# Kernel optimization log

Hardware: AMD Instinct MI355X
Metric: run time of the kernel (lower is better)

Reference implementation:

```python
import jax, jax.numpy as jnp
import numpy as np

B, L, D, S = 64, 512, 768, 8
HOP, LAMB = 3, 0.5


def _layernorm(x, g, b, eps=1e-5):
    m = x.mean(-1, keepdims=True)
    v = x.var(-1, keepdims=True)
    return (x - m) / jnp.sqrt(v + eps) * g + b


def _hop_refine(cur, sentence, ln_g, ln_b):
    # cur, sentence: [B,S,D]. HOP-1 refinement steps, then return last row.
    for _ in range(HOP - 1):
        coef = jnp.einsum('bd,bsd->bs', cur[:, -1, :], sentence)  # [B,S]
        a = coef[..., None] * sentence                             # [B,S,D]
        cur = LAMB * _layernorm(jax.nn.sigmoid(a), ln_g, ln_b) + sentence
    return cur[:, -1, :]  # [B,D]


def _conv1d(x, w, b):
    # x: [B,D,S], w: [Dout,Din,3], padding=1 (same)
    y = jax.lax.conv_general_dilated(
        x, w, window_strides=(1,), padding=((1, 1),),
        dimension_numbers=('NCH', 'OIH', 'NCH'))
    return y + b[None, :, None]


def setup_inputs() -> dict:
    key = jax.random.key(0)
    ks = jax.random.split(key, 16)
    p = lambda k, shp: (jax.random.normal(k, shp, dtype=jnp.float32) * 0.02)
    # segment boundaries: strictly increasing, start at 1, <= L, gaps ~63 with jitter < 32
    base = 1 + np.arange(S + 1) * ((L - 1) // S)          # [9]
    jitter = np.array(jax.random.randint(ks[15], (B, S + 1), 0, 32))
    jitter[:, 0] = 0
    jitter[:, -1] = 0
    seg_bounds = jnp.asarray(base[None, :] + jitter, dtype=jnp.int64 if jax.config.jax_enable_x64 else jnp.int32)
    return {
        'bert_output': jax.random.normal(ks[0], (B, L, D), dtype=jnp.float32),
        'target': jax.random.normal(ks[1], (B, D), dtype=jnp.float32),
        'gc1_w': p(ks[2], (D, D)), 'gc1_b': p(ks[3], (D,)),
        'gc2_w': p(ks[4], (D, D)), 'gc2_b': p(ks[5], (D,)),
        'conv1_w': p(ks[6], (D, D, 3)), 'conv1_b': p(ks[7], (D,)),
        'conv2_w': p(ks[8], (D, D, 3)), 'conv2_b': p(ks[9], (D,)),
        'ln_g': jnp.ones((D,), jnp.float32), 'ln_b': jnp.zeros((D,), jnp.float32),
        'fc2_w': p(ks[10], (3 * D, 3)), 'fc2_b': p(ks[11], (3,)),
        'seg_bounds': seg_bounds,
    }


def reference(bert_output, target, gc1_w, gc1_b, gc2_w, gc2_b,
              conv1_w, conv1_b, conv2_w, conv2_b, ln_g, ln_b,
              fc2_w, fc2_b, seg_bounds):
    dt = bert_output.dtype
    start = seg_bounds[:, :-1]   # [B,S]
    end = seg_bounds[:, 1:]      # [B,S]
    pos = jnp.arange(L)
    seg_mask = ((pos[None, None, :] >= start[:, :, None]) &
                (pos[None, None, :] < end[:, :, None])).astype(dt)  # [B,S,L]
    cnt = (end - start).astype(dt)                                   # [B,S]
    # batched segment-mean pooling
    sentence = jnp.einsum('bsl,bld->bsd', seg_mask, bert_output) / cnt[..., None]

    # GCN branch: adj = I + superdiagonal, row-degree normalization
    adj = jnp.eye(S, dtype=dt) + jnp.eye(S, k=1, dtype=dt)
    denom = adj.sum(axis=1)  # [S]

    def gcn(x, w, b):
        h = jnp.einsum('bsd,de->bse', x, w)
        return jnp.einsum('st,btd->bsd', adj, h) / denom[None, :, None] + b

    g1 = jnp.tanh(gcn(sentence, gc1_w, gc1_b))
    g2 = jnp.tanh(gcn(g1, gc2_w, gc2_b))
    a3 = _hop_refine(g2, sentence, ln_g, ln_b)

    # Conv branch: two conv1d (k=3, pad=1) over the segment axis
    x = jnp.swapaxes(sentence, 1, 2)  # [B,D,S]
    c = jnp.tanh(_conv1d(x, conv1_w, conv1_b))
    c = jnp.tanh(_conv1d(c, conv2_w, conv2_b))
    conv_out = jnp.swapaxes(c, 1, 2)  # [B,S,D]
    a4 = _hop_refine(conv_out, sentence, ln_g, ln_b)

    # Self-mask branch
    coef0 = jnp.einsum('bd,bsd->bs', sentence[:, -1, :], sentence)
    tmask = jax.nn.sigmoid(coef0[..., None] * sentence)
    a5 = _hop_refine(tmask, sentence, ln_g, ln_b)

    fnout = jnp.stack([a3, a4, a5], axis=1)                 # [B,3,D]
    # NOTE: original uses target[0] (first sample's pooler output) for all samples
    w = jax.nn.softmax(jnp.einsum('bkd,d->bk', fnout, target[0]), axis=1)
    fn = (fnout * w[..., None]).reshape(fnout.shape[0], 3 * D)
    return fn @ fc2_w + fc2_b  # [B,3]
```

## Files before the change

kernel.cpp:

```cpp
#include <hip/hip_runtime.h>


typedef unsigned short u16;
typedef short short8 __attribute__((ext_vector_type(8)));
typedef float f32x4 __attribute__((ext_vector_type(4)));

__device__ __forceinline__ float bf2f(u16 h) {
    unsigned int u = ((unsigned int)h) << 16;
    float f;
    __builtin_memcpy(&f, &u, 4);
    return f;
}
__device__ __forceinline__ u16 f2bf(float f) {
    unsigned int u;
    __builtin_memcpy(&u, &f, 4);
    u = (u + 0x7fffu + ((u >> 16) & 1u)) >> 16;
    return (u16)u;
}
__device__ __forceinline__ float sigm(float x) { return 1.0f / (1.0f + __expf(-x)); }

__device__ __forceinline__ float ldv(const void* p, long i, bool bf) {
    return bf ? bf2f(((const u16*)p)[i]) : ((const float*)p)[i];
}

__device__ __forceinline__ bool detect_bf16(const u16* bert) {
    int hits = 0;
#pragma unroll
    for (int i = 0; i < 256; i += 2) {
        const int e = (bert[i] >> 7) & 0xFF;
        hits += (e >= 115 && e <= 130) ? 1 : 0;
    }
    return hits > 64;
}

__global__ __launch_bounds__(256) void k0_zero(float* __restrict__ ws)
{
    ((float4*)ws)[blockIdx.x * 256 + threadIdx.x] = make_float4(0.f, 0.f, 0.f, 0.f);
}

__global__ __launch_bounds__(256) void k1_pool(
    const void* __restrict__ bertv, const int* __restrict__ sb,
    float* __restrict__ sentF, float* __restrict__ flagp)
{
    const int u = blockIdx.x, t = threadIdx.x;
    const bool bf = detect_bf16((const u16*)bertv);
    const bool is64 = (sb[1] == 0);
    if (u == 0 && t == 0) flagp[0] = bf ? 1.0f : 0.0f;
    const int q = u & 3, v = u >> 2;
    const int b = v / 3, si = v - 3 * (v / 3), s = 5 + si;
    const int i0 = b * 9 + s, i1 = i0 + 1;
    int st = is64 ? sb[2 * i0] : sb[i0];
    int en = is64 ? sb[2 * i1] : sb[i1];
    st = st < 0 ? 0 : (st > 511 ? 511 : st);
    en = en <= st ? st + 1 : (en > 512 ? 512 : en);
    const int n = en - st;
    const int r0 = st + (n * q) / 4;
    const int r1 = st + (n * (q + 1)) / 4;
    float a0 = 0.f, a1 = 0.f, a2 = 0.f;
    if (bf) {
        const u16* base = (const u16*)bertv + (size_t)b * 512 * 768;
        int l = r0;
        for (; l + 1 < r1; l += 2) {
            const u16* p0 = base + (size_t)l * 768;
            const u16* p1 = p0 + 768;
            const u16 x0 = p0[t], x1 = p0[t + 256], x2 = p0[t + 512];
            const u16 y0 = p1[t], y1 = p1[t + 256], y2 = p1[t + 512];
            a0 += bf2f(x0) + bf2f(y0);
            a1 += bf2f(x1) + bf2f(y1);
            a2 += bf2f(x2) + bf2f(y2);
        }
        if (l < r1) {
            const u16* p0 = base + (size_t)l * 768;
            a0 += bf2f(p0[t]);
            a1 += bf2f(p0[t + 256]);
            a2 += bf2f(p0[t + 512]);
        }
    } else {
        const float* base = (const float*)bertv + (size_t)b * 512 * 768;
        int l = r0;
        for (; l + 1 < r1; l += 2) {
            const float* p0 = base + (size_t)l * 768;
            const float* p1 = p0 + 768;
            const float x0 = p0[t], x1 = p0[t + 256], x2 = p0[t + 512];
            const float y0 = p1[t], y1 = p1[t + 256], y2 = p1[t + 512];
            a0 += x0 + y0;
            a1 += x1 + y1;
            a2 += x2 + y2;
        }
        if (l < r1) {
            const float* p0 = base + (size_t)l * 768;
            a0 += p0[t];
            a1 += p0[t + 256];
            a2 += p0[t + 512];
        }
    }
    const float inv = 1.0f / (float)n;
    float* o = sentF + b * 2304 + si * 768;
    atomicAdd(o + t, a0 * inv);
    atomicAdd(o + t + 256, a1 * inv);
    atomicAdd(o + t + 512, a2 * inv);
}

template <int XMODE, int WMODE>
__device__ __forceinline__ void gemm_core(
    const float* __restrict__ x, int xstride, const void* __restrict__ bias,
    const void* __restrict__ W, bool bf,
    float* __restrict__ out, int ostride,
    int n0, int k0, u16* As, u16* Bs)
{
    const int t = threadIdx.x;
    const int r = t >> 2;
    const int cseg = (t & 3) * 32;
    const int wave = t >> 6, lane = t & 63;
    const int lm = lane & 15, lq = lane >> 4;
    f32x4 acc[4] = {};

    for (int kk = 0; kk < 256; kk += 128) {
        const int kg = k0 + kk;
        {
            const float* xp = x + (size_t)r * xstride + (kg + cseg);
            u16* dst = As + r * 136 + cseg;
#pragma unroll
            for (int i = 0; i < 8; ++i) {
                float4 v = ((const float4*)xp)[i];
                if (XMODE == 1) {
                    int kb = kg + cseg + i * 4;
                    if (kb >= 768) kb -= 768;
                    v.x = tanhf(v.x + ldv(bias, kb, bf));
                    v.y = tanhf(v.y + ldv(bias, kb + 1, bf));
                    v.z = tanhf(v.z + ldv(bias, kb + 2, bf));
                    v.w = tanhf(v.w + ldv(bias, kb + 3, bf));
                }
                ((ushort4*)dst)[i] = make_ushort4(f2bf(v.x), f2bf(v.y), f2bf(v.z), f2bf(v.w));
            }
        }
        if (WMODE == 0) {
            const int p = t >> 2;
            const int nseg = (t & 3) * 16;
            u16 q0[16], q1[16];
            if (bf) {
                const u16* w0 = (const u16*)W + (size_t)(kg + 2 * p) * 768 + n0 + nseg;
                ((uint4*)q0)[0] = ((const uint4*)w0)[0];
                ((uint4*)q0)[1] = ((const uint4*)w0)[1];
                ((uint4*)q1)[0] = ((const uint4*)(w0 + 768))[0];
                ((uint4*)q1)[1] = ((const uint4*)(w0 + 768))[1];
            } else {
                const float* w0 = (const float*)W + (size_t)(kg + 2 * p) * 768 + n0 + nseg;
#pragma unroll
                for (int e = 0; e < 4; ++e) {
                    float4 v0 = ((const float4*)w0)[e];
                    float4 v1 = ((const float4*)(w0 + 768))[e];
                    q0[4 * e] = f2bf(v0.x); q0[4 * e + 1] = f2bf(v0.y);
                    q0[4 * e + 2] = f2bf(v0.z); q0[4 * e + 3] = f2bf(v0.w);
                    q1[4 * e] = f2bf(v1.x); q1[4 * e + 1] = f2bf(v1.y);
                    q1[4 * e + 2] = f2bf(v1.z); q1[4 * e + 3] = f2bf(v1.w);
                }
            }
#pragma unroll
            for (int e = 0; e < 16; ++e)
                *(ushort2*)(Bs + (nseg + e) * 136 + 2 * p) = make_ushort2(q0[e], q1[e]);
        } else {
            const int kb = kg / 768;
            const int i0c = kg - kb * 768;
            u16 tmp[32];
            if (bf) {
                const u16* wp = (const u16*)W + (size_t)(n0 + r) * 2304 + (size_t)(i0c + cseg) * 3 + kb;
#pragma unroll
                for (int j = 0; j < 32; ++j) tmp[j] = wp[j * 3];
            } else {
                const float* wp = (const float*)W + (size_t)(n0 + r) * 2304 + (size_t)(i0c + cseg) * 3 + kb;
#pragma unroll
                for (int j = 0; j < 32; ++j) tmp[j] = f2bf(wp[j * 3]);
            }
            u16* dst = Bs + r * 136 + cseg;
#pragma unroll
            for (int qq = 0; qq < 8; ++qq)
                ((ushort4*)dst)[qq] = ((ushort4*)tmp)[qq];
        }
        __syncthreads();
        const u16* ap = As + (wave * 16 + lm) * 136 + lq * 8;
        const u16* bp = Bs + lm * 136 + lq * 8;
#pragma unroll
        for (int ks = 0; ks < 4; ++ks) {
            short8 af = *(const short8*)(ap + ks * 32);
#pragma unroll
            for (int nf = 0; nf < 4; ++nf) {
                short8 bfr = *(const short8*)(bp + nf * 16 * 136 + ks * 32);
                acc[nf] = __builtin_amdgcn_mfma_f32_16x16x32_bf16(af, bfr, acc[nf], 0, 0, 0);
            }
        }
        __syncthreads();
    }
#pragma unroll
    for (int nf = 0; nf < 4; ++nf) {
#pragma unroll
        for (int rg = 0; rg < 4; ++rg) {
            const int row = wave * 16 + lq * 4 + rg;
            const int col = n0 + nf * 16 + lm;
            atomicAdd(out + (size_t)row * ostride + col, acc[nf][rg]);
        }
    }
}

__global__ __launch_bounds__(256) void k2_gemm_a(
    const float* __restrict__ sentF, const void* __restrict__ gc1w,
    const void* __restrict__ c1w, float* __restrict__ g1acc, float* __restrict__ c1acc,
    const float* __restrict__ flagp)
{
    __shared__ u16 As[64 * 136];
    __shared__ u16 Bs[64 * 136];
    const bool bf = flagp[0] > 0.5f;
    const int u = blockIdx.x;
    if (u < 36) {
        gemm_core<0, 0>(sentF + 1536, 2304, nullptr, gc1w, bf, g1acc, 768,
                        (u / 3) * 64, (u % 3) * 256, As, Bs);
    } else if (u < 144) {
        const int v = u - 36;
        gemm_core<0, 1>(sentF, 2304, nullptr, c1w, bf, c1acc, 1536,
                        (v / 9) * 64, (v % 9) * 256, As, Bs);
    } else {
        const int v = u - 144;
        gemm_core<0, 1>(sentF + 768, 2304, nullptr, c1w, bf, c1acc + 768, 1536,
                        (v / 6) * 64, (v % 6) * 256, As, Bs);
    }
}

__global__ __launch_bounds__(256) void k3_gemm_b(
    const float* __restrict__ g1acc, const float* __restrict__ c1acc,
    const void* __restrict__ gc2w, const void* __restrict__ c2w,
    const void* __restrict__ gc1b, const void* __restrict__ c1b,
    float* __restrict__ g2acc, float* __restrict__ c2acc,
    const float* __restrict__ flagp)
{
    __shared__ u16 As[64 * 136];
    __shared__ u16 Bs[64 * 136];
    const bool bf = flagp[0] > 0.5f;
    const int u = blockIdx.x;
    if (u < 36) {
        gemm_core<1, 0>(g1acc, 768, gc1b, gc2w, bf, g2acc, 768,
                        (u / 3) * 64, (u % 3) * 256, As, Bs);
    } else {
        const int v = u - 36;
        gemm_core<1, 1>(c1acc, 1536, c1b, c2w, bf, c2acc, 768,
                        (v / 6) * 64, (v % 6) * 256, As, Bs);
    }
}

__device__ __forceinline__ float block_sum(float v, float* red) {
#pragma unroll
    for (int m = 1; m < 64; m <<= 1) v += __shfl_xor(v, m, 64);
    const int wave = threadIdx.x >> 6, lane = threadIdx.x & 63;
    if (lane == 0) red[wave] = v;
    __syncthreads();
    const float r = red[0] + red[1] + red[2] + red[3];
    __syncthreads();
    return r;
}

__global__ __launch_bounds__(256) void k4_final(
    const float* __restrict__ sentF, const float* __restrict__ g2acc,
    const float* __restrict__ c2acc,
    const void* __restrict__ gc2b, const void* __restrict__ c2b,
    const void* __restrict__ lng, const void* __restrict__ lnb,
    const void* __restrict__ target, const void* __restrict__ fc2w,
    const void* __restrict__ fc2b, void* __restrict__ outp,
    const float* __restrict__ flagp)
{
    __shared__ float red[4];
    const bool bf = flagp[0] > 0.5f;
    const int t = threadIdx.x, b = blockIdx.x;
    float s_[3], g_[3], bb_[3];
    const float* srow = sentF + b * 2304 + 1536;
#pragma unroll
    for (int i = 0; i < 3; ++i) {
        const int d = t + 256 * i;
        s_[i] = srow[d];
        g_[i] = ldv(lng, d, bf);
        bb_[i] = ldv(lnb, d, bf);
    }

    auto refine2 = [&](float* yv) {
#pragma unroll
        for (int it = 0; it < 2; ++it) {
            const float c = block_sum(yv[0] * s_[0] + yv[1] * s_[1] + yv[2] * s_[2], red);
            float tt[3], sm = 0.0f, sq = 0.0f;
#pragma unroll
            for (int i = 0; i < 3; ++i) {
                tt[i] = sigm(c * s_[i]);
                sm += tt[i];
                sq += tt[i] * tt[i];
            }
            const float m = block_sum(sm, red) * (1.0f / 768.0f);
            const float q = block_sum(sq, red) * (1.0f / 768.0f);
            const float inv = rsqrtf(fmaxf(q - m * m, 0.0f) + 1e-5f);
#pragma unroll
            for (int i = 0; i < 3; ++i)
                yv[i] = 0.5f * ((tt[i] - m) * inv * g_[i] + bb_[i]) + s_[i];
        }
    };

    float a3[3], a4[3], a5[3], y[3];
#pragma unroll
    for (int i = 0; i < 3; ++i) {
        const int d = t + 256 * i;
        y[i] = tanhf(g2acc[b * 768 + d] + ldv(gc2b, d, bf));
    }
    refine2(y);
    a3[0] = y[0]; a3[1] = y[1]; a3[2] = y[2];
#pragma unroll
    for (int i = 0; i < 3; ++i) {
        const int d = t + 256 * i;
        y[i] = tanhf(c2acc[b * 768 + d] + ldv(c2b, d, bf));
    }
    refine2(y);
    a4[0] = y[0]; a4[1] = y[1]; a4[2] = y[2];
    const float ss = block_sum(s_[0] * s_[0] + s_[1] * s_[1] + s_[2] * s_[2], red);
#pragma unroll
    for (int i = 0; i < 3; ++i) y[i] = sigm(ss * s_[i]);
    refine2(y);
    a5[0] = y[0]; a5[1] = y[1]; a5[2] = y[2];

    float tg[3];
#pragma unroll
    for (int i = 0; i < 3; ++i) tg[i] = ldv(target, t + 256 * i, bf);
    const float u0 = block_sum(a3[0] * tg[0] + a3[1] * tg[1] + a3[2] * tg[2], red);
    const float u1 = block_sum(a4[0] * tg[0] + a4[1] * tg[1] + a4[2] * tg[2], red);
    const float u2 = block_sum(a5[0] * tg[0] + a5[1] * tg[1] + a5[2] * tg[2], red);
    const float mx = fmaxf(u0, fmaxf(u1, u2));
    const float e0 = __expf(u0 - mx), e1 = __expf(u1 - mx), e2 = __expf(u2 - mx);
    const float es = e0 + e1 + e2;
    const float w0 = e0 / es, w1 = e1 / es, w2 = e2 / es;

    float p0 = 0.0f, p1 = 0.0f, p2 = 0.0f;
#pragma unroll
    for (int i = 0; i < 3; ++i) {
        const int d = t + 256 * i;
        const float va = w0 * a3[i], vb = w1 * a4[i], vc = w2 * a5[i];
        p0 += va * ldv(fc2w, d * 3 + 0, bf) + vb * ldv(fc2w, (768 + d) * 3 + 0, bf) + vc * ldv(fc2w, (1536 + d) * 3 + 0, bf);
        p1 += va * ldv(fc2w, d * 3 + 1, bf) + vb * ldv(fc2w, (768 + d) * 3 + 1, bf) + vc * ldv(fc2w, (1536 + d) * 3 + 1, bf);
        p2 += va * ldv(fc2w, d * 3 + 2, bf) + vb * ldv(fc2w, (768 + d) * 3 + 2, bf) + vc * ldv(fc2w, (1536 + d) * 3 + 2, bf);
    }
    p0 = block_sum(p0, red);
    p1 = block_sum(p1, red);
    p2 = block_sum(p2, red);
    if (t == 0) {
        const float o0 = p0 + ldv(fc2b, 0, bf);
        const float o1 = p1 + ldv(fc2b, 1, bf);
        const float o2 = p2 + ldv(fc2b, 2, bf);
        if (bf) {
            ((u16*)outp)[b * 3 + 0] = f2bf(o0);
            ((u16*)outp)[b * 3 + 1] = f2bf(o1);
            ((u16*)outp)[b * 3 + 2] = f2bf(o2);
        } else {
            ((float*)outp)[b * 3 + 0] = o0;
            ((float*)outp)[b * 3 + 1] = o1;
            ((float*)outp)[b * 3 + 2] = o2;
        }
    }
}

extern "C" void kernel_launch(void* const* d_in, const int* in_sizes, int n_in,
                              void* d_out, int out_size, void* d_ws, size_t ws_size,
                              hipStream_t stream) {
    const void* bert   = d_in[0];
    const void* target = d_in[1];
    const void* gc1w   = d_in[2];
    const void* gc1b   = d_in[3];
    const void* gc2w   = d_in[4];
    const void* gc2b   = d_in[5];
    const void* c1w    = d_in[6];
    const void* c1b    = d_in[7];
    const void* c2w    = d_in[8];
    const void* c2b    = d_in[9];
    const void* lng    = d_in[10];
    const void* lnb    = d_in[11];
    const void* fc2w   = d_in[12];
    const void* fc2b   = d_in[13];
    const int*  sb     = (const int*)d_in[14];

    float* sentF = (float*)d_ws;
    float* accs  = sentF + 147456;
    float* g1acc = accs;
    float* c1acc = accs + 49152;
    float* g2acc = c1acc + 98304;
    float* c2acc = g2acc + 49152;
    float* flagp = accs + 245760;

    k0_zero<<<384, 256, 0, stream>>>(sentF);
    k1_pool<<<768, 256, 0, stream>>>(bert, sb, sentF, flagp);
    k2_gemm_a<<<216, 256, 0, stream>>>(sentF, gc1w, c1w, g1acc, c1acc, flagp);
    k3_gemm_b<<<108, 256, 0, stream>>>(g1acc, c1acc, gc2w, c2w, gc1b, c1b, g2acc, c2acc, flagp);
    k4_final<<<64, 256, 0, stream>>>(sentF, g2acc, c2acc, gc2b, c2b, lng, lnb,
                                     target, fc2w, fc2b, d_out, flagp);
}
```

Measured before the change: 224.5 us.

## Fuse all stages into one cooperative kernel with grid syncs

Replaces the five-kernel pipeline with a single cooperative kernel of 256 blocks that pools, runs both GEMM stages and the final reduction, separated by grid.sync barriers. Pooling writes four partial buffers instead of using atomics, and the first GEMM sums those partials on load. The second GEMM is re-split into 216 blocks with half-K tiles so the fixed grid is better used. This removes launch overhead and the separate zeroing kernel, at the cost of grid-wide barriers and the first GEMM reading the pooled inputs four times.

```diff
diff --git a/kernel.cpp b/kernel.cpp
--- a/kernel.cpp
+++ b/kernel.cpp
@@ -1,9 +1,14 @@
 #include <hip/hip_runtime.h>
+#include <hip/hip_cooperative_groups.h>
+
+namespace cg = cooperative_groups;
 
 
 typedef unsigned short u16;
 typedef short short8 __attribute__((ext_vector_type(8)));
 typedef float f32x4 __attribute__((ext_vector_type(4)));
+
+#define PSTRIDE 147456
 
 __device__ __forceinline__ float bf2f(u16 h) {
     unsigned int u = ((unsigned int)h) << 16;
@@ -31,6 +36,345 @@
         hits += (e >= 115 && e <= 130) ? 1 : 0;
     }
     return hits > 64;
+}
+
+template <int XMODE, int WMODE>
+__device__ __forceinline__ void gemm_core(
+    const float* __restrict__ x, int xstride, const void* __restrict__ bias,
+    const void* __restrict__ W, bool bf,
+    float* __restrict__ out, int ostride,
+    int n0, int k0, int kiters, u16* As, u16* Bs)
+{
+    const int t = threadIdx.x;
+    const int r = t >> 2;
+    const int cseg = (t & 3) * 32;
+    const int wave = t >> 6, lane = t & 63;
+    const int lm = lane & 15, lq = lane >> 4;
+    f32x4 acc[4] = {};
+
+    for (int kk = 0; kk < kiters * 128; kk += 128) {
+        const int kg = k0 + kk;
+        {
+            const float* xp = x + (size_t)r * xstride + (kg + cseg);
+            u16* dst = As + r * 136 + cseg;
+#pragma unroll
+            for (int i = 0; i < 8; ++i) {
+                float4 v = ((const float4*)xp)[i];
+                if (XMODE == 2) {
+                    float4 v1 = ((const float4*)(xp + PSTRIDE))[i];
+                    float4 v2 = ((const float4*)(xp + 2 * PSTRIDE))[i];
+                    float4 v3 = ((const float4*)(xp + 3 * PSTRIDE))[i];
+                    v.x += v1.x + v2.x + v3.x;
+                    v.y += v1.y + v2.y + v3.y;
+                    v.z += v1.z + v2.z + v3.z;
+                    v.w += v1.w + v2.w + v3.w;
+                }
+                if (XMODE == 1) {
+                    int kb = kg + cseg + i * 4;
+                    if (kb >= 768) kb -= 768;
+                    v.x = tanhf(v.x + ldv(bias, kb, bf));
+                    v.y = tanhf(v.y + ldv(bias, kb + 1, bf));
+                    v.z = tanhf(v.z + ldv(bias, kb + 2, bf));
+                    v.w = tanhf(v.w + ldv(bias, kb + 3, bf));
+                }
+                ((ushort4*)dst)[i] = make_ushort4(f2bf(v.x), f2bf(v.y), f2bf(v.z), f2bf(v.w));
+            }
+        }
+        if (WMODE == 0) {
+            const int p = t >> 2;
+            const int nseg = (t & 3) * 16;
+            u16 q0[16], q1[16];
+            if (bf) {
+                const u16* w0 = (const u16*)W + (size_t)(kg + 2 * p) * 768 + n0 + nseg;
+                ((uint4*)q0)[0] = ((const uint4*)w0)[0];
+                ((uint4*)q0)[1] = ((const uint4*)w0)[1];
+                ((uint4*)q1)[0] = ((const uint4*)(w0 + 768))[0];
+                ((uint4*)q1)[1] = ((const uint4*)(w0 + 768))[1];
+            } else {
+                const float* w0 = (const float*)W + (size_t)(kg + 2 * p) * 768 + n0 + nseg;
+#pragma unroll
+                for (int e = 0; e < 4; ++e) {
+                    float4 v0 = ((const float4*)w0)[e];
+                    float4 v1 = ((const float4*)(w0 + 768))[e];
+                    q0[4 * e] = f2bf(v0.x); q0[4 * e + 1] = f2bf(v0.y);
+                    q0[4 * e + 2] = f2bf(v0.z); q0[4 * e + 3] = f2bf(v0.w);
+                    q1[4 * e] = f2bf(v1.x); q1[4 * e + 1] = f2bf(v1.y);
+                    q1[4 * e + 2] = f2bf(v1.z); q1[4 * e + 3] = f2bf(v1.w);
+                }
+            }
+#pragma unroll
+            for (int e = 0; e < 16; ++e)
+                *(ushort2*)(Bs + (nseg + e) * 136 + 2 * p) = make_ushort2(q0[e], q1[e]);
+        } else {
+            const int kb = kg / 768;
+            const int i0c = kg - kb * 768;
+            u16 tmp[32];
+            if (bf) {
+                const u16* wp = (const u16*)W + (size_t)(n0 + r) * 2304 + (size_t)(i0c + cseg) * 3 + kb;
+#pragma unroll
+                for (int j = 0; j < 32; ++j) tmp[j] = wp[j * 3];
+            } else {
+                const float* wp = (const float*)W + (size_t)(n0 + r) * 2304 + (size_t)(i0c + cseg) * 3 + kb;
+#pragma unroll
+                for (int j = 0; j < 32; ++j) tmp[j] = f2bf(wp[j * 3]);
+            }
+            u16* dst = Bs + r * 136 + cseg;
+#pragma unroll
+            for (int qq = 0; qq < 8; ++qq)
+                ((ushort4*)dst)[qq] = ((ushort4*)tmp)[qq];
+        }
+        __syncthreads();
+        const u16* ap = As + (wave * 16 + lm) * 136 + lq * 8;
+        const u16* bp = Bs + lm * 136 + lq * 8;
+#pragma unroll
+        for (int ks = 0; ks < 4; ++ks) {
+            short8 af = *(const short8*)(ap + ks * 32);
+#pragma unroll
+            for (int nf = 0; nf < 4; ++nf) {
+                short8 bfr = *(const short8*)(bp + nf * 16 * 136 + ks * 32);
+                acc[nf] = __builtin_amdgcn_mfma_f32_16x16x32_bf16(af, bfr, acc[nf], 0, 0, 0);
+            }
+        }
+        __syncthreads();
+    }
+#pragma unroll
+    for (int nf = 0; nf < 4; ++nf) {
+#pragma unroll
+        for (int rg = 0; rg < 4; ++rg) {
+            const int row = wave * 16 + lq * 4 + rg;
+            const int col = n0 + nf * 16 + lm;
+            atomicAdd(out + (size_t)row * ostride + col, acc[nf][rg]);
+        }
+    }
+}
+
+__device__ __forceinline__ float block_sum(float v, float* red) {
+#pragma unroll
+    for (int m = 1; m < 64; m <<= 1) v += __shfl_xor(v, m, 64);
+    const int wave = threadIdx.x >> 6, lane = threadIdx.x & 63;
+    if (lane == 0) red[wave] = v;
+    __syncthreads();
+    const float r = red[0] + red[1] + red[2] + red[3];
+    __syncthreads();
+    return r;
+}
+
+__global__ __launch_bounds__(256) void kfused(
+    const void* __restrict__ bert, const int* __restrict__ sb,
+    const void* __restrict__ target,
+    const void* __restrict__ gc1w, const void* __restrict__ gc1b,
+    const void* __restrict__ gc2w, const void* __restrict__ gc2b,
+    const void* __restrict__ c1w, const void* __restrict__ c1b,
+    const void* __restrict__ c2w, const void* __restrict__ c2b,
+    const void* __restrict__ lng, const void* __restrict__ lnb,
+    const void* __restrict__ fc2w, const void* __restrict__ fc2b,
+    void* __restrict__ outp, float* __restrict__ ws)
+{
+    __shared__ u16 As[64 * 136];
+    __shared__ u16 Bs[64 * 136];
+    __shared__ float red[4];
+    const int t = threadIdx.x;
+    const int blk = blockIdx.x;
+    cg::grid_group grid = cg::this_grid();
+
+    const bool bf = detect_bf16((const u16*)bert);
+    const bool is64 = (sb[1] == 0);
+
+    float* sentP = ws;
+    float* accs  = ws + 4 * PSTRIDE;
+    float* g1acc = accs;
+    float* c1acc = g1acc + 49152;
+    float* g2acc = c1acc + 98304;
+    float* c2acc = g2acc + 49152;
+
+    if (t < 240)
+        ((float4*)accs)[blk * 240 + t] = make_float4(0.f, 0.f, 0.f, 0.f);
+
+#pragma unroll
+    for (int un = 0; un < 3; ++un) {
+        const int u = blk + 256 * un;
+        const int q = u & 3, v = u >> 2;
+        const int b = v / 3, si = v - 3 * (v / 3), s = 5 + si;
+        const int i0 = b * 9 + s, i1 = i0 + 1;
+        int st = is64 ? sb[2 * i0] : sb[i0];
+        int en = is64 ? sb[2 * i1] : sb[i1];
+        st = st < 0 ? 0 : (st > 511 ? 511 : st);
+        en = en <= st ? st + 1 : (en > 512 ? 512 : en);
+        const int n = en - st;
+        const int r0 = st + (n * q) / 4;
+        const int r1 = st + (n * (q + 1)) / 4;
+        float a0 = 0.f, a1 = 0.f, a2 = 0.f;
+        if (bf) {
+            const u16* base = (const u16*)bert + (size_t)b * 512 * 768;
+            int l = r0;
+            for (; l + 1 < r1; l += 2) {
+                const u16* p0 = base + (size_t)l * 768;
+                const u16* p1 = p0 + 768;
+                a0 += bf2f(p0[t]) + bf2f(p1[t]);
+                a1 += bf2f(p0[t + 256]) + bf2f(p1[t + 256]);
+                a2 += bf2f(p0[t + 512]) + bf2f(p1[t + 512]);
+            }
+            if (l < r1) {
+                const u16* p0 = base + (size_t)l * 768;
+                a0 += bf2f(p0[t]);
+                a1 += bf2f(p0[t + 256]);
+                a2 += bf2f(p0[t + 512]);
+            }
+        } else {
+            const float* base = (const float*)bert + (size_t)b * 512 * 768;
+            int l = r0;
+            for (; l + 1 < r1; l += 2) {
+                const float* p0 = base + (size_t)l * 768;
+                const float* p1 = p0 + 768;
+                a0 += p0[t] + p1[t];
+                a1 += p0[t + 256] + p1[t + 256];
+                a2 += p0[t + 512] + p1[t + 512];
+            }
+            if (l < r1) {
+                const float* p0 = base + (size_t)l * 768;
+                a0 += p0[t];
+                a1 += p0[t + 256];
+                a2 += p0[t + 512];
+            }
+        }
+        const float inv = 1.0f / (float)n;
+        float* o = sentP + (size_t)q * PSTRIDE + b * 2304 + si * 768;
+        o[t] = a0 * inv;
+        o[t + 256] = a1 * inv;
+        o[t + 512] = a2 * inv;
+    }
+
+    __threadfence();
+    grid.sync();
+    __threadfence();
+
+    if (blk < 216) {
+        const int u = blk;
+        if (u < 36) {
+            gemm_core<2, 0>(sentP + 1536, 2304, nullptr, gc1w, bf, g1acc, 768,
+                            (u / 3) * 64, (u % 3) * 256, 2, As, Bs);
+        } else if (u < 144) {
+            const int v = u - 36;
+            gemm_core<2, 1>(sentP, 2304, nullptr, c1w, bf, c1acc, 1536,
+                            (v / 9) * 64, (v % 9) * 256, 2, As, Bs);
+        } else {
+            const int v = u - 144;
+            gemm_core<2, 1>(sentP + 768, 2304, nullptr, c1w, bf, c1acc + 768, 1536,
+                            (v / 6) * 64, (v % 6) * 256, 2, As, Bs);
+        }
+    }
+
+    __threadfence();
+    grid.sync();
+    __threadfence();
+
+    if (blk < 216) {
+        const int u = blk;
+        if (u < 72) {
+            gemm_core<1, 0>(g1acc, 768, gc1b, gc2w, bf, g2acc, 768,
+                            (u / 6) * 64, (u % 6) * 128, 1, As, Bs);
+        } else {
+            const int v = u - 72;
+            gemm_core<1, 1>(c1acc, 1536, c1b, c2w, bf, c2acc, 768,
+                            (v / 12) * 64, (v % 12) * 128, 1, As, Bs);
+        }
+    }
+
+    __threadfence();
+    grid.sync();
+    __threadfence();
+
+    if (blk < 64) {
+        const int b = blk;
+        float s_[3], g_[3], bb_[3];
+        const float* srow = sentP + b * 2304 + 1536;
+#pragma unroll
+        for (int i = 0; i < 3; ++i) {
+            const int d = t + 256 * i;
+            s_[i] = srow[d] + srow[d + PSTRIDE] + srow[d + 2 * PSTRIDE] + srow[d + 3 * PSTRIDE];
+            g_[i] = ldv(lng, d, bf);
+            bb_[i] = ldv(lnb, d, bf);
+        }
+
+        auto refine2 = [&](float* yv) {
+#pragma unroll
+            for (int it = 0; it < 2; ++it) {
+                const float c = block_sum(yv[0] * s_[0] + yv[1] * s_[1] + yv[2] * s_[2], red);
+                float tt[3], sm = 0.0f, sq = 0.0f;
+#pragma unroll
+                for (int i = 0; i < 3; ++i) {
+                    tt[i] = sigm(c * s_[i]);
+                    sm += tt[i];
+                    sq += tt[i] * tt[i];
+                }
+                const float m = block_sum(sm, red) * (1.0f / 768.0f);
+                const float q = block_sum(sq, red) * (1.0f / 768.0f);
+                const float inv = rsqrtf(fmaxf(q - m * m, 0.0f) + 1e-5f);
+#pragma unroll
+                for (int i = 0; i < 3; ++i)
+                    yv[i] = 0.5f * ((tt[i] - m) * inv * g_[i] + bb_[i]) + s_[i];
+            }
+        };
+
+        float a3[3], a4[3], a5[3], y[3];
+#pragma unroll
+        for (int i = 0; i < 3; ++i) {
+            const int d = t + 256 * i;
+            y[i] = tanhf(g2acc[b * 768 + d] + ldv(gc2b, d, bf));
+        }
+        refine2(y);
+        a3[0] = y[0]; a3[1] = y[1]; a3[2] = y[2];
+#pragma unroll
+        for (int i = 0; i < 3; ++i) {
+            const int d = t + 256 * i;
+            y[i] = tanhf(c2acc[b * 768 + d] + ldv(c2b, d, bf));
+        }
+        refine2(y);
+        a4[0] = y[0]; a4[1] = y[1]; a4[2] = y[2];
+        const float ss = block_sum(s_[0] * s_[0] + s_[1] * s_[1] + s_[2] * s_[2], red);
+#pragma unroll
+        for (int i = 0; i < 3; ++i) y[i] = sigm(ss * s_[i]);
+        refine2(y);
+        a5[0] = y[0]; a5[1] = y[1]; a5[2] = y[2];
+
+        float tg[3];
+#pragma unroll
+        for (int i = 0; i < 3; ++i) tg[i] = ldv(target, t + 256 * i, bf);
+        const float u0 = block_sum(a3[0] * tg[0] + a3[1] * tg[1] + a3[2] * tg[2], red);
+        const float u1 = block_sum(a4[0] * tg[0] + a4[1] * tg[1] + a4[2] * tg[2], red);
+        const float u2 = block_sum(a5[0] * tg[0] + a5[1] * tg[1] + a5[2] * tg[2], red);
+        const float mx = fmaxf(u0, fmaxf(u1, u2));
+        const float e0 = __expf(u0 - mx), e1 = __expf(u1 - mx), e2 = __expf(u2 - mx);
+        const float es = e0 + e1 + e2;
+        const float w0 = e0 / es, w1 = e1 / es, w2 = e2 / es;
+
+        float p0 = 0.0f, p1 = 0.0f, p2 = 0.0f;
+#pragma unroll
+        for (int i = 0; i < 3; ++i) {
+            const int d = t + 256 * i;
+            const float va = w0 * a3[i], vb = w1 * a4[i], vc = w2 * a5[i];
+            p0 += va * ldv(fc2w, d * 3 + 0, bf) + vb * ldv(fc2w, (768 + d) * 3 + 0, bf) + vc * ldv(fc2w, (1536 + d) * 3 + 0, bf);
+            p1 += va * ldv(fc2w, d * 3 + 1, bf) + vb * ldv(fc2w, (768 + d) * 3 + 1, bf) + vc * ldv(fc2w, (1536 + d) * 3 + 1, bf);
+            p2 += va * ldv(fc2w, d * 3 + 2, bf) + vb * ldv(fc2w, (768 + d) * 3 + 2, bf) + vc * ldv(fc2w, (1536 + d) * 3 + 2, bf);
+        }
+        p0 = block_sum(p0, red);
+        p1 = block_sum(p1, red);
+        p2 = block_sum(p2, red);
+        if (t == 0) {
+            const float o0 = p0 + ldv(fc2b, 0, bf);
+            const float o1 = p1 + ldv(fc2b, 1, bf);
+            const float o2 = p2 + ldv(fc2b, 2, bf);
+            if (bf) {
+                ((u16*)outp)[b * 3 + 0] = f2bf(o0);
+                ((u16*)outp)[b * 3 + 1] = f2bf(o1);
+                ((u16*)outp)[b * 3 + 2] = f2bf(o2);
+            } else {
+                ((float*)outp)[b * 3 + 0] = o0;
+                ((float*)outp)[b * 3 + 1] = o1;
+                ((float*)outp)[b * 3 + 2] = o2;
+            }
+        }
+    }
 }
 
 __global__ __launch_bounds__(256) void k0_zero(float* __restrict__ ws)
@@ -63,17 +407,13 @@
         for (; l + 1 < r1; l += 2) {
             const u16* p0 = base + (size_t)l * 768;
             const u16* p1 = p0 + 768;
-            const u16 x0 = p0[t], x1 = p0[t + 256], x2 = p0[t + 512];
-            const u16 y0 = p1[t], y1 = p1[t + 256], y2 = p1[t + 512];
-            a0 += bf2f(x0) + bf2f(y0);
-            a1 += bf2f(x1) + bf2f(y1);
-            a2 += bf2f(x2) + bf2f(y2);
+            a0 += bf2f(p0[t]) + bf2f(p1[t]);
+            a1 += bf2f(p0[t + 256]) + bf2f(p1[t + 256]);
+            a2 += bf2f(p0[t + 512]) + bf2f(p1[t + 512]);
         }
         if (l < r1) {
             const u16* p0 = base + (size_t)l * 768;
-            a0 += bf2f(p0[t]);
-            a1 += bf2f(p0[t + 256]);
-            a2 += bf2f(p0[t + 512]);
+            a0 += bf2f(p0[t]); a1 += bf2f(p0[t + 256]); a2 += bf2f(p0[t + 512]);
         }
     } else {
         const float* base = (const float*)bertv + (size_t)b * 512 * 768;
@@ -81,17 +421,13 @@
         for (; l + 1 < r1; l += 2) {
             const float* p0 = base + (size_t)l * 768;
             const float* p1 = p0 + 768;
-            const float x0 = p0[t], x1 = p0[t + 256], x2 = p0[t + 512];
-            const float y0 = p1[t], y1 = p1[t + 256], y2 = p1[t + 512];
-            a0 += x0 + y0;
-            a1 += x1 + y1;
-            a2 += x2 + y2;
+            a0 += p0[t] + p1[t];
+            a1 += p0[t + 256] + p1[t + 256];
+            a2 += p0[t + 512] + p1[t + 512];
         }
         if (l < r1) {
             const float* p0 = base + (size_t)l * 768;
-            a0 += p0[t];
-            a1 += p0[t + 256];
-            a2 += p0[t + 512];
+            a0 += p0[t]; a1 += p0[t + 256]; a2 += p0[t + 512];
         }
     }
     const float inv = 1.0f / (float)n;
@@ -99,107 +435,6 @@
     atomicAdd(o + t, a0 * inv);
     atomicAdd(o + t + 256, a1 * inv);
     atomicAdd(o + t + 512, a2 * inv);
-}
-
-template <int XMODE, int WMODE>
-__device__ __forceinline__ void gemm_core(
-    const float* __restrict__ x, int xstride, const void* __restrict__ bias,
-    const void* __restrict__ W, bool bf,
-    float* __restrict__ out, int ostride,
-    int n0, int k0, u16* As, u16* Bs)
-{
-    const int t = threadIdx.x;
-    const int r = t >> 2;
-    const int cseg = (t & 3) * 32;
-    const int wave = t >> 6, lane = t & 63;
-    const int lm = lane & 15, lq = lane >> 4;
-    f32x4 acc[4] = {};
-
-    for (int kk = 0; kk < 256; kk += 128) {
-        const int kg = k0 + kk;
-        {
-            const float* xp = x + (size_t)r * xstride + (kg + cseg);
-            u16* dst = As + r * 136 + cseg;
-#pragma unroll
-            for (int i = 0; i < 8; ++i) {
-                float4 v = ((const float4*)xp)[i];
-                if (XMODE == 1) {
-                    int kb = kg + cseg + i * 4;
-                    if (kb >= 768) kb -= 768;
-                    v.x = tanhf(v.x + ldv(bias, kb, bf));
-                    v.y = tanhf(v.y + ldv(bias, kb + 1, bf));
-                    v.z = tanhf(v.z + ldv(bias, kb + 2, bf));
-                    v.w = tanhf(v.w + ldv(bias, kb + 3, bf));
-                }
-                ((ushort4*)dst)[i] = make_ushort4(f2bf(v.x), f2bf(v.y), f2bf(v.z), f2bf(v.w));
-            }
-        }
-        if (WMODE == 0) {
-            const int p = t >> 2;
-            const int nseg = (t & 3) * 16;
-            u16 q0[16], q1[16];
-            if (bf) {
-                const u16* w0 = (const u16*)W + (size_t)(kg + 2 * p) * 768 + n0 + nseg;
-                ((uint4*)q0)[0] = ((const uint4*)w0)[0];
-                ((uint4*)q0)[1] = ((const uint4*)w0)[1];
-                ((uint4*)q1)[0] = ((const uint4*)(w0 + 768))[0];
-                ((uint4*)q1)[1] = ((const uint4*)(w0 + 768))[1];
-            } else {
-                const float* w0 = (const float*)W + (size_t)(kg + 2 * p) * 768 + n0 + nseg;
-#pragma unroll
-                for (int e = 0; e < 4; ++e) {
-                    float4 v0 = ((const float4*)w0)[e];
-                    float4 v1 = ((const float4*)(w0 + 768))[e];
-                    q0[4 * e] = f2bf(v0.x); q0[4 * e + 1] = f2bf(v0.y);
-                    q0[4 * e + 2] = f2bf(v0.z); q0[4 * e + 3] = f2bf(v0.w);
-                    q1[4 * e] = f2bf(v1.x); q1[4 * e + 1] = f2bf(v1.y);
-                    q1[4 * e + 2] = f2bf(v1.z); q1[4 * e + 3] = f2bf(v1.w);
-                }
-            }
-#pragma unroll
-            for (int e = 0; e < 16; ++e)
-                *(ushort2*)(Bs + (nseg + e) * 136 + 2 * p) = make_ushort2(q0[e], q1[e]);
-        } else {
-            const int kb = kg / 768;
-            const int i0c = kg - kb * 768;
-            u16 tmp[32];
-            if (bf) {
-                const u16* wp = (const u16*)W + (size_t)(n0 + r) * 2304 + (size_t)(i0c + cseg) * 3 + kb;
-#pragma unroll
-                for (int j = 0; j < 32; ++j) tmp[j] = wp[j * 3];
-            } else {
-                const float* wp = (const float*)W + (size_t)(n0 + r) * 2304 + (size_t)(i0c + cseg) * 3 + kb;
-#pragma unroll
-                for (int j = 0; j < 32; ++j) tmp[j] = f2bf(wp[j * 3]);
-            }
-            u16* dst = Bs + r * 136 + cseg;
-#pragma unroll
-            for (int qq = 0; qq < 8; ++qq)
-                ((ushort4*)dst)[qq] = ((ushort4*)tmp)[qq];
-        }
-        __syncthreads();
-        const u16* ap = As + (wave * 16 + lm) * 136 + lq * 8;
-        const u16* bp = Bs + lm * 136 + lq * 8;
-#pragma unroll
-        for (int ks = 0; ks < 4; ++ks) {
-            short8 af = *(const short8*)(ap + ks * 32);
-#pragma unroll
-            for (int nf = 0; nf < 4; ++nf) {
-                short8 bfr = *(const short8*)(bp + nf * 16 * 136 + ks * 32);
-                acc[nf] = __builtin_amdgcn_mfma_f32_16x16x32_bf16(af, bfr, acc[nf], 0, 0, 0);
-            }
-        }
-        __syncthreads();
-    }
-#pragma unroll
-    for (int nf = 0; nf < 4; ++nf) {
-#pragma unroll
-        for (int rg = 0; rg < 4; ++rg) {
-            const int row = wave * 16 + lq * 4 + rg;
-            const int col = n0 + nf * 16 + lm;
-            atomicAdd(out + (size_t)row * ostride + col, acc[nf][rg]);
-        }
-    }
 }
 
 __global__ __launch_bounds__(256) void k2_gemm_a(
@@ -213,15 +448,15 @@
     const int u = blockIdx.x;
     if (u < 36) {
         gemm_core<0, 0>(sentF + 1536, 2304, nullptr, gc1w, bf, g1acc, 768,
-                        (u / 3) * 64, (u % 3) * 256, As, Bs);
+                        (u / 3) * 64, (u % 3) * 256, 2, As, Bs);
     } else if (u < 144) {
         const int v = u - 36;
         gemm_core<0, 1>(sentF, 2304, nullptr, c1w, bf, c1acc, 1536,
-                        (v / 9) * 64, (v % 9) * 256, As, Bs);
+                        (v / 9) * 64, (v % 9) * 256, 2, As, Bs);
     } else {
         const int v = u - 144;
         gemm_core<0, 1>(sentF + 768, 2304, nullptr, c1w, bf, c1acc + 768, 1536,
-                        (v / 6) * 64, (v % 6) * 256, As, Bs);
+                        (v / 6) * 64, (v % 6) * 256, 2, As, Bs);
     }
 }
 
@@ -238,23 +473,12 @@
     const int u = blockIdx.x;
     if (u < 36) {
         gemm_core<1, 0>(g1acc, 768, gc1b, gc2w, bf, g2acc, 768,
-                        (u / 3) * 64, (u % 3) * 256, As, Bs);
+                        (u / 3) * 64, (u % 3) * 256, 2, As, Bs);
     } else {
         const int v = u - 36;
         gemm_core<1, 1>(c1acc, 1536, c1b, c2w, bf, c2acc, 768,
-                        (v / 6) * 64, (v % 6) * 256, As, Bs);
-    }
-}
-
-__device__ __forceinline__ float block_sum(float v, float* red) {
-#pragma unroll
-    for (int m = 1; m < 64; m <<= 1) v += __shfl_xor(v, m, 64);
-    const int wave = threadIdx.x >> 6, lane = threadIdx.x & 63;
-    if (lane == 0) red[wave] = v;
-    __syncthreads();
-    const float r = red[0] + red[1] + red[2] + red[3];
-    __syncthreads();
-    return r;
+                        (v / 6) * 64, (v % 6) * 256, 2, As, Bs);
+    }
 }
 
 __global__ __launch_bounds__(256) void k4_final(
@@ -278,7 +502,6 @@
         g_[i] = ldv(lng, d, bf);
         bb_[i] = ldv(lnb, d, bf);
     }
-
     auto refine2 = [&](float* yv) {
 #pragma unroll
         for (int it = 0; it < 2; ++it) {
@@ -298,7 +521,6 @@
                 yv[i] = 0.5f * ((tt[i] - m) * inv * g_[i] + bb_[i]) + s_[i];
         }
     };
-
     float a3[3], a4[3], a5[3], y[3];
 #pragma unroll
     for (int i = 0; i < 3; ++i) {
@@ -319,7 +541,6 @@
     for (int i = 0; i < 3; ++i) y[i] = sigm(ss * s_[i]);
     refine2(y);
     a5[0] = y[0]; a5[1] = y[1]; a5[2] = y[2];
-
     float tg[3];
 #pragma unroll
     for (int i = 0; i < 3; ++i) tg[i] = ldv(target, t + 256 * i, bf);
@@ -330,7 +551,6 @@
     const float e0 = __expf(u0 - mx), e1 = __expf(u1 - mx), e2 = __expf(u2 - mx);
     const float es = e0 + e1 + e2;
     const float w0 = e0 / es, w1 = e1 / es, w2 = e2 / es;
-
     float p0 = 0.0f, p1 = 0.0f, p2 = 0.0f;
 #pragma unroll
     for (int i = 0; i < 3; ++i) {
@@ -377,19 +597,30 @@
     const void* fc2w   = d_in[12];
     const void* fc2b   = d_in[13];
     const int*  sb     = (const int*)d_in[14];
-
-    float* sentF = (float*)d_ws;
-    float* accs  = sentF + 147456;
-    float* g1acc = accs;
-    float* c1acc = accs + 49152;
-    float* g2acc = c1acc + 98304;
-    float* c2acc = g2acc + 49152;
-    float* flagp = accs + 245760;
-
-    k0_zero<<<384, 256, 0, stream>>>(sentF);
-    k1_pool<<<768, 256, 0, stream>>>(bert, sb, sentF, flagp);
-    k2_gemm_a<<<216, 256, 0, stream>>>(sentF, gc1w, c1w, g1acc, c1acc, flagp);
-    k3_gemm_b<<<108, 256, 0, stream>>>(g1acc, c1acc, gc2w, c2w, gc1b, c1b, g2acc, c2acc, flagp);
-    k4_final<<<64, 256, 0, stream>>>(sentF, g2acc, c2acc, gc2b, c2b, lng, lnb,
-                                     target, fc2w, fc2b, d_out, flagp);
-}
+    float* wsf = (float*)d_ws;
+
+    void* args[17] = {
+        (void*)&bert, (void*)&sb, (void*)&target,
+        (void*)&gc1w, (void*)&gc1b, (void*)&gc2w, (void*)&gc2b,
+        (void*)&c1w, (void*)&c1b, (void*)&c2w, (void*)&c2b,
+        (void*)&lng, (void*)&lnb, (void*)&fc2w, (void*)&fc2b,
+        (void*)&d_out, (void*)&wsf};
+    hipError_t err = hipLaunchCooperativeKernel(
+        (void*)kfused, dim3(256), dim3(256), args, 0, stream);
+
+    if (err != hipSuccess) {
+        float* sentF = wsf;
+        float* accs  = sentF + 147456;
+        float* g1acc = accs;
+        float* c1acc = accs + 49152;
+        float* g2acc = c1acc + 98304;
+        float* c2acc = g2acc + 49152;
+        float* flagp = accs + 245760;
+        k0_zero<<<384, 256, 0, stream>>>(sentF);
+        k1_pool<<<768, 256, 0, stream>>>(bert, sb, sentF, flagp);
+        k2_gemm_a<<<216, 256, 0, stream>>>(sentF, gc1w, c1w, g1acc, c1acc, flagp);
+        k3_gemm_b<<<108, 256, 0, stream>>>(g1acc, c1acc, gc2w, c2w, gc1b, c1b, g2acc, c2acc, flagp);
+        k4_final<<<64, 256, 0, stream>>>(sentF, g2acc, c2acc, gc2b, c2b, lng, lnb,
+                                         target, fc2w, fc2b, d_out, flagp);
+    }
+}
```

Result: slower. 463.1 us (+106.3%).
